# Kernel tuning notes

Hardware: AMD Instinct MI355X
Metric: run time of the kernel (lower is better)

The kernel has to match this reference:

```python
import jax, jax.numpy as jnp
import numpy as np

DIM = 1024
DIM_MEDIA = 1024
DIM_HEAD = 64
HEADS = 8
INNER = DIM_HEAD * HEADS  # 512
B, N_TOK, N_LAT = 4, 4096, 1024
LN_EPS = 1e-5


def setup_inputs() -> dict:
    key = jax.random.key(0)
    ks = jax.random.split(key, 6)
    x = jax.random.normal(ks[0], (B, N_TOK, DIM), dtype=jnp.float32)
    media = jax.random.normal(ks[1], (B, N_LAT, DIM_MEDIA), dtype=jnp.float32)
    media_mask = jax.random.randint(ks[2], (B, N_LAT), 0, 2).astype(bool)
    media_mask = media_mask.at[:, 0].set(True)  # avoid fully-masked rows (NaN softmax)
    ln_gamma = jnp.ones((DIM,), jnp.float32)
    ln_beta = jnp.zeros((DIM,), jnp.float32)
    Wq = jax.random.normal(ks[3], (DIM, INNER), jnp.float32) * (DIM ** -0.5)
    Wkv = jax.random.normal(ks[4], (DIM_MEDIA, 2 * INNER), jnp.float32) * (DIM_MEDIA ** -0.5)
    Wout = jax.random.normal(ks[5], (INNER, DIM), jnp.float32) * (INNER ** -0.5)
    return {"x": x, "media": media, "media_mask": media_mask,
            "ln_gamma": ln_gamma, "ln_beta": ln_beta,
            "Wq": Wq, "Wkv": Wkv, "Wout": Wout}


def reference(x, media, media_mask, ln_gamma, ln_beta, Wq, Wkv, Wout):
    scale = DIM_HEAD ** -0.5
    # LayerNorm over last dim
    mu = jnp.mean(x, axis=-1, keepdims=True)
    var = jnp.mean(jnp.square(x - mu), axis=-1, keepdims=True)
    xn = (x - mu) * jax.lax.rsqrt(var + LN_EPS) * ln_gamma + ln_beta

    q = (xn @ Wq) * scale                      # [b, n, inner]
    kv = media @ Wkv                           # [b, m, 2*inner]
    k, v = jnp.split(kv, 2, axis=-1)

    def to_heads(t):
        b, n, _ = t.shape
        return t.reshape(b, n, HEADS, DIM_HEAD).transpose(0, 2, 1, 3)  # b h n d

    q, k, v = to_heads(q), to_heads(k), to_heads(v)

    sim = jnp.einsum('bhid,bhjd->bhij', q, k)  # [b, h, n_tok, n_lat]
    neg_inf = jnp.float32(-jnp.inf)
    sim = jnp.where(media_mask[:, None, None, :], sim, neg_inf)
    sim = sim - jax.lax.stop_gradient(jnp.max(sim, axis=-1, keepdims=True))
    attn = jax.nn.softmax(sim, axis=-1)
    out = jnp.einsum('bhij,bhjd->bhid', attn, v)  # [b, h, n_tok, d]
    out = out.transpose(0, 2, 1, 3).reshape(out.shape[0], out.shape[2], INNER)
    return out @ Wout  # [b, n_tok, dim]
```

## Files before the change

kernel.cpp:

```cpp
#include <hip/hip_runtime.h>
#include <hip/hip_bf16.h>

typedef short bf16x8 __attribute__((ext_vector_type(8)));
typedef float f32x4 __attribute__((ext_vector_type(4)));
typedef unsigned short u16;

#define AS1 __attribute__((address_space(1)))
#define AS3 __attribute__((address_space(3)))

#define DIM     1024
#define INNER   512
#define HEADS   8
#define DHEAD   64
#define BATCH   4
#define NTOK    4096
#define NLAT    1024
#define M_X     (BATCH*NTOK)
#define M_MED   (BATCH*NLAT)
#define LN_EPS  1e-5f
#define QSCALE  (0.125f * 1.44269504f)

__device__ __forceinline__ float b2f(u16 h) {
    union { unsigned u; float f; } v; v.u = ((unsigned)h) << 16; return v.f;
}
__device__ __forceinline__ u16 f2b(float f) {
    union { float f; unsigned u; } v; v.f = f;
    unsigned r = v.u + 0x7fff + ((v.u >> 16) & 1);
    return (u16)(r >> 16);
}
__device__ __forceinline__ unsigned cvt_pk(float lo, float hi) {
    unsigned r;
    asm("v_cvt_pk_bf16_f32 %0, %1, %2" : "=v"(r) : "v"(lo), "v"(hi));
    return r;
}

__launch_bounds__(256)
__global__ void detect_kernel(const unsigned* __restrict__ xw, const unsigned* __restrict__ maskw,
                              unsigned* __restrict__ flags) {
    __shared__ int s_bad, s_byte;
    if (threadIdx.x == 0) { s_bad = 0; s_byte = 0; }
    __syncthreads();
    unsigned w = xw[threadIdx.x];
    int bad = 0;
    #pragma unroll
    for (int h = 0; h < 2; h++) {
        unsigned el = (h ? (w >> 16) : w) & 0xFFFFu;
        unsigned ef = (el >> 7) & 0xFFu;
        if (!((ef >= 64u && ef < 192u) || (el & 0x7FFFu) == 0u)) bad = 1;
    }
    if (bad) atomicOr(&s_bad, 1);
    for (int i = threadIdx.x; i < NLAT; i += 256)
        if (maskw[i] > 1u) { atomicOr(&s_byte, 1); break; }
    __syncthreads();
    if (threadIdx.x == 0) { flags[0] = s_bad ? 0u : 1u; flags[1] = s_byte ? 1u : 0u; }
}

#define PREP_BLOCKS 6156

__device__ __forceinline__ void do_transpose(const void* in, u16* out, int R, int C,
                                             int bx, int by, bool bf, u16 (*t)[33],
                                             const void* gv) {
    int c0 = bx * 32, r0 = by * 32;
    int tid = threadIdx.x;
    int r = tid >> 3, cb = (tid & 7) * 4;
    size_t base = (size_t)(r0 + r) * C + c0 + cb;
    u16 e0, e1, e2, e3;
    if (bf) {
        ushort4 a = *(const ushort4*)((const u16*)in + base);
        if (gv) {
            float sc = b2f(((const u16*)gv)[r0 + r]);
            e0 = f2b(b2f(a.x) * sc); e1 = f2b(b2f(a.y) * sc);
            e2 = f2b(b2f(a.z) * sc); e3 = f2b(b2f(a.w) * sc);
        } else {
            e0 = a.x; e1 = a.y; e2 = a.z; e3 = a.w;
        }
    } else {
        float4 a = *(const float4*)((const float*)in + base);
        float sc = gv ? ((const float*)gv)[r0 + r] : 1.f;
        e0 = f2b(a.x * sc); e1 = f2b(a.y * sc); e2 = f2b(a.z * sc); e3 = f2b(a.w * sc);
    }
    t[r][cb] = e0; t[r][cb + 1] = e1; t[r][cb + 2] = e2; t[r][cb + 3] = e3;
    __syncthreads();
    ushort4 o;
    o.x = t[cb + 0][r]; o.y = t[cb + 1][r]; o.z = t[cb + 2][r]; o.w = t[cb + 3][r];
    *(ushort4*)(out + (size_t)(c0 + r) * R + r0 + cb) = o;
}

__launch_bounds__(256)
__global__ void prep_kernel(const void* __restrict__ x, const void* __restrict__ g,
                            const void* __restrict__ bt, u16* __restrict__ xc,
                            const void* __restrict__ media, u16* __restrict__ media_c,
                            const void* __restrict__ mask, int* __restrict__ map,
                            int* __restrict__ cnt,
                            const void* __restrict__ Wq, u16* __restrict__ WqT,
                            const void* __restrict__ Wkv, u16* __restrict__ WkvT,
                            const void* __restrict__ Wout, u16* __restrict__ WoutT,
                            float2* __restrict__ stats, float* __restrict__ Gv,
                            float* __restrict__ Bv,
                            const unsigned* __restrict__ flags) {
    __shared__ int wsumI[4];
    __shared__ u16 t[32][33];
    __shared__ float rg[4][64], rb[4][64];
    bool bf = flags[0] != 0;
    int bid = blockIdx.x, tid = threadIdx.x;

    if (bid < 2048) {
        int w = tid >> 6, lane = tid & 63;
        int row0 = (bid << 3) + (w << 1);
        float v[2][16];
        if (bf) {
            const u16* xr = (const u16*)x + (size_t)row0 * DIM;
            bf16x8 a[4];
            #pragma unroll
            for (int rr = 0; rr < 2; rr++)
                #pragma unroll
                for (int i = 0; i < 2; i++)
                    a[rr * 2 + i] = *(const bf16x8*)(xr + (size_t)rr * DIM + (lane + 64 * i) * 8);
            #pragma unroll
            for (int rr = 0; rr < 2; rr++)
                #pragma unroll
                for (int i = 0; i < 2; i++)
                    #pragma unroll
                    for (int j = 0; j < 8; j++)
                        v[rr][i * 8 + j] = b2f((u16)a[rr * 2 + i][j]);
        } else {
            const float* xr = (const float*)x + (size_t)row0 * DIM;
            float4 a[8];
            #pragma unroll
            for (int rr = 0; rr < 2; rr++)
                #pragma unroll
                for (int i = 0; i < 4; i++)
                    a[rr * 4 + i] = *(const float4*)(xr + (size_t)rr * DIM + (lane + 64 * i) * 4);
            #pragma unroll
            for (int rr = 0; rr < 2; rr++)
                #pragma unroll
                for (int i = 0; i < 4; i++) {
                    v[rr][i * 4 + 0] = a[rr * 4 + i].x; v[rr][i * 4 + 1] = a[rr * 4 + i].y;
                    v[rr][i * 4 + 2] = a[rr * 4 + i].z; v[rr][i * 4 + 3] = a[rr * 4 + i].w;
                }
        }
        float s[2] = {0.f, 0.f}, s2[2] = {0.f, 0.f};
        #pragma unroll
        for (int rr = 0; rr < 2; rr++)
            #pragma unroll
            for (int i = 0; i < 16; i++) { s[rr] += v[rr][i]; s2[rr] += v[rr][i] * v[rr][i]; }
        #pragma unroll
        for (int m = 1; m < 64; m <<= 1) {
            #pragma unroll
            for (int rr = 0; rr < 2; rr++) {
                s[rr] += __shfl_xor(s[rr], m);
                s2[rr] += __shfl_xor(s2[rr], m);
            }
        }
        #pragma unroll
        for (int rr = 0; rr < 2; rr++) {
            float mu = s[rr] * (1.f / DIM);
            float var = s2[rr] * (1.f / DIM) - mu * mu;
            float inv = rsqrtf(fmaxf(var, 0.f) + LN_EPS);
            if (lane == 0) stats[row0 + rr] = make_float2(inv * QSCALE, inv * mu * QSCALE);
        }
        if (!bf) {
            u16* orow = xc + (size_t)row0 * DIM;
            #pragma unroll
            for (int rr = 0; rr < 2; rr++)
                #pragma unroll
                for (int i = 0; i < 4; i++) {
                    ushort4 o;
                    o.x = f2b(v[rr][i * 4 + 0]); o.y = f2b(v[rr][i * 4 + 1]);
                    o.z = f2b(v[rr][i * 4 + 2]); o.w = f2b(v[rr][i * 4 + 3]);
                    *(ushort4*)(orow + (size_t)rr * DIM + (lane + 64 * i) * 4) = o;
                }
        }
    } else if (bid < 4096) {
        if (bf) return;
        size_t i = ((size_t)(bid - 2048) * 256 + tid) * 8;
        const float* s = (const float*)media + i;
        float4 a = *(const float4*)s, b = *(const float4*)(s + 4);
        u16 o[8] = {f2b(a.x), f2b(a.y), f2b(a.z), f2b(a.w),
                    f2b(b.x), f2b(b.y), f2b(b.z), f2b(b.w)};
        *(bf16x8*)(media_c + i) = *(bf16x8*)o;
    } else if (bid < 4100) {
        int b = bid - 4096;
        bool bytes = flags[1] != 0;
        int v[4];
        if (bytes) {
            unsigned wd = ((const unsigned*)mask)[b * 256 + tid];
            #pragma unroll
            for (int i = 0; i < 4; i++) v[i] = ((wd >> (8 * i)) & 0xFFu) ? 1 : 0;
        } else {
            int4 m4 = ((const int4*)mask)[b * 256 + tid];
            v[0] = m4.x != 0; v[1] = m4.y != 0; v[2] = m4.z != 0; v[3] = m4.w != 0;
        }
        int tsum = v[0] + v[1] + v[2] + v[3];
        int lane = tid & 63, w = tid >> 6;
        int incl = tsum;
        #pragma unroll
        for (int off = 1; off < 64; off <<= 1) {
            int tt = __shfl_up(incl, off);
            if (lane >= off) incl += tt;
        }
        if (lane == 63) wsumI[w] = incl;
        __syncthreads();
        int base = 0;
        for (int k = 0; k < w; k++) base += wsumI[k];
        int slot = base + incl - tsum;
        int gbase = b * NLAT + tid * 4;
        #pragma unroll
        for (int i = 0; i < 4; i++) map[gbase + i] = v[i] ? slot++ : -1;
        if (tid == 0) cnt[b] = wsumI[0] + wsumI[1] + wsumI[2] + wsumI[3];
    } else if (bid < 4612) {
        int idx = bid - 4100;
        do_transpose(Wq, WqT, DIM, INNER, idx & 15, idx >> 4, bf, t, g);
    } else if (bid < 5636) {
        int idx = bid - 4612;
        do_transpose(Wkv, WkvT, DIM, DIM, idx & 31, idx >> 5, bf, t, nullptr);
    } else if (bid < 6148) {
        int idx = bid - 5636;
        do_transpose(Wout, WoutT, INNER, DIM, idx & 31, idx >> 5, bf, t, nullptr);
    } else {
        int idx = bid - 6148;
        int col = idx * 64 + (tid & 63), kq = tid >> 6;
        float ag = 0.f, ab = 0.f;
        if (bf) {
            const u16* W = (const u16*)Wq;
            const u16* gg = (const u16*)g;
            const u16* bb = (const u16*)bt;
            for (int k = kq * 256; k < kq * 256 + 256; k += 4) {
                #pragma unroll
                for (int u = 0; u < 4; u++) {
                    float wv = b2f(W[(size_t)(k + u) * INNER + col]);
                    ag += b2f(gg[k + u]) * wv;
                    ab += b2f(bb[k + u]) * wv;
                }
            }
        } else {
            const float* W = (const float*)Wq;
            const float* gg = (const float*)g;
            const float* bb = (const float*)bt;
            for (int k = kq * 256; k < kq * 256 + 256; k += 4) {
                #pragma unroll
                for (int u = 0; u < 4; u++) {
                    float wv = W[(size_t)(k + u) * INNER + col];
                    ag += gg[k + u] * wv;
                    ab += bb[k + u] * wv;
                }
            }
        }
        rg[kq][tid & 63] = ag; rb[kq][tid & 63] = ab;
        __syncthreads();
        if (kq == 0) {
            int c = tid & 63;
            Gv[col] = rg[0][c] + rg[1][c] + rg[2][c] + rg[3][c];
            Bv[col] = (rb[0][c] + rb[1][c] + rb[2][c] + rb[3][c]) * QSCALE;
        }
    }
}

__device__ __forceinline__ void gemm_body(const u16* __restrict__ A, const u16* __restrict__ Bt,
                                          u16* __restrict__ C, float* __restrict__ Cf,
                                          int Ndim, int K, float scale, int mode,
                                          u16* __restrict__ vT, const int* __restrict__ map,
                                          bool outbf, int n0, int m0, u16* As, u16* Bs,
                                          const float2* __restrict__ stats,
                                          const float* __restrict__ Gv,
                                          const float* __restrict__ Bv) {
    int tid = threadIdx.x;
    int w = tid >> 6, lane = tid & 63, quad = lane >> 4, l15 = lane & 15;
    int wm = (w >> 1) * 64, wn = (w & 1) * 64;
    f32x4 acc[4][4] = {};
    int rowInSeg = lane >> 2;
    int colB = (((lane & 3) ^ ((lane >> 3) & 3))) * 8;
    for (int k0 = 0; k0 < K; k0 += 32) {
        __syncthreads();
        #pragma unroll
        for (int i = 0; i < 2; i++) {
            int seg = w * 2 + i;
            int row = seg * 16 + rowInSeg;
            __builtin_amdgcn_global_load_lds(
                (const AS1 void*)(A + (size_t)(m0 + row) * K + k0 + colB),
                (AS3 void*)(As + seg * 512), 16, 0, 0);
            __builtin_amdgcn_global_load_lds(
                (const AS1 void*)(Bt + (size_t)(n0 + row) * K + k0 + colB),
                (AS3 void*)(Bs + seg * 512), 16, 0, 0);
        }
        __syncthreads();
        int sw = quad ^ ((l15 >> 1) & 3);
        bf16x8 af[4], bfr[4];
        #pragma unroll
        for (int i = 0; i < 4; i++)
            af[i] = *(bf16x8*)&As[(wm + i * 16 + l15) * 32 + sw * 8];
        #pragma unroll
        for (int j = 0; j < 4; j++)
            bfr[j] = *(bf16x8*)&Bs[(wn + j * 16 + l15) * 32 + sw * 8];
        #pragma unroll
        for (int i = 0; i < 4; i++)
            #pragma unroll
            for (int j = 0; j < 4; j++)
                acc[i][j] = __builtin_amdgcn_mfma_f32_16x16x32_bf16(af[i], bfr[j], acc[i][j], 0, 0, 0);
    }
    #pragma unroll
    for (int i = 0; i < 4; i++)
        #pragma unroll
        for (int j = 0; j < 4; j++)
            #pragma unroll
            for (int r = 0; r < 4; r++) {
                int row = m0 + wm + i * 16 + quad * 4 + r;
                int col = n0 + wn + j * 16 + l15;
                if (mode == 0) {
                    float2 st = stats[row];
                    float val = st.x * acc[i][j][r] - st.y * Gv[col] + Bv[col];
                    C[(size_t)row * Ndim + col] = f2b(val);
                } else if (mode == 1) {
                    float val = acc[i][j][r];
                    int b = row >> 10, jj = row & 1023;
                    int slot = map[(b << 10) + jj];
                    if (slot >= 0) {
                        if (col < INNER) {
                            C[((size_t)(b << 10) + slot) * INNER + col] = f2b(val);
                        } else {
                            int c = col - INNER;
                            int h = c >> 6, d = c & 63;
                            vT[(((size_t)(b * HEADS + h) * 64 + d) << 10) + slot] = f2b(val);
                        }
                    }
                } else {
                    float val = acc[i][j][r] * scale;
                    if (outbf) C[(size_t)row * Ndim + col] = f2b(val);
                    else       Cf[(size_t)row * Ndim + col] = val;
                }
            }
}

__launch_bounds__(256, 3)
__global__ void gemm128(const u16* __restrict__ A, const u16* __restrict__ Bt,
                        u16* __restrict__ C, float* __restrict__ Cf, int Ndim, int K,
                        float scale, int mode, u16* __restrict__ vT,
                        const int* __restrict__ map,
                        const unsigned* __restrict__ flags) {
    __shared__ __align__(16) u16 As[128 * 32];
    __shared__ __align__(16) u16 Bs[128 * 32];
    bool outbf = (mode != 2) || (flags[0] != 0);
    gemm_body(A, Bt, C, Cf, Ndim, K, scale, mode, vT, map, outbf,
              blockIdx.x * 128, blockIdx.y * 128, As, Bs,
              (const float2*)nullptr, (const float*)nullptr, (const float*)nullptr);
}

__launch_bounds__(256, 3)
__global__ void gemm_qkv(const void* __restrict__ x, const u16* __restrict__ xc,
                         const u16* __restrict__ WqT, u16* __restrict__ qb,
                         const void* __restrict__ media, const u16* __restrict__ media_c,
                         const u16* __restrict__ WkvT,
                         u16* __restrict__ Kb, u16* __restrict__ vT,
                         const int* __restrict__ map,
                         const float2* __restrict__ stats, const float* __restrict__ Gv,
                         const float* __restrict__ Bv,
                         const unsigned* __restrict__ flags) {
    __shared__ __align__(16) u16 As[128 * 32];
    __shared__ __align__(16) u16 Bs[128 * 32];
    bool bf = flags[0] != 0;
    int bid = blockIdx.x;
    if (bid < 512) {
        const u16* A = bf ? (const u16*)x : xc;
        gemm_body(A, WqT, qb, (float*)nullptr, INNER, DIM, 1.0f, 0,
                  (u16*)nullptr, (int*)nullptr, true,
                  (bid & 3) * 128, (bid >> 2) * 128, As, Bs, stats, Gv, Bv);
    } else {
        int id = bid - 512;
        const u16* A = bf ? (const u16*)media : media_c;
        gemm_body(A, WkvT, Kb, (float*)nullptr, DIM, DIM, 1.0f, 1,
                  vT, map, true,
                  (id & 7) * 128, (id >> 3) * 128, As, Bs,
                  (const float2*)nullptr, (const float*)nullptr, (const float*)nullptr);
    }
}

__launch_bounds__(256, 6)
__global__ void flash_kernel(const u16* __restrict__ q, const u16* __restrict__ Kc,
                             const u16* __restrict__ vTc, const int* __restrict__ cntp,
                             u16* __restrict__ attn_out) {
    __shared__ __align__(16) u16 Ks[64 * 64];
    __shared__ __align__(16) u16 Vts[64 * 64];
    __shared__ __align__(16) u16 Ps[4][16 * 68];
    int bh = blockIdx.x >> 6;
    int qt = blockIdx.x & 63;
    int b = bh >> 3, h = bh & 7;
    int tid = threadIdx.x, w = tid >> 6, lane = tid & 63, quad = lane >> 4, l15 = lane & 15;
    int qrow0 = qt * 64 + w * 16;
    int cnt = cntp[b];

    size_t qbase = ((size_t)(b * NTOK) + qrow0 + l15) * INNER + h * 64;
    bf16x8 qf[2];
    qf[0] = *(const bf16x8*)(q + qbase + quad * 8);
    qf[1] = *(const bf16x8*)(q + qbase + 32 + quad * 8);

    f32x4 Oacc[4] = {};
    float lsum = 0.f;
    int ld_row = lane >> 3;
    int ld_col = ((lane & 7) ^ ld_row) * 8;

    for (int jt = 0; jt < cnt; jt += 64) {
        __syncthreads();
        #pragma unroll
        for (int i = 0; i < 2; i++) {
            int seg = w * 2 + i;
            int j = jt + seg * 8 + ld_row;
            __builtin_amdgcn_global_load_lds(
                (const AS1 void*)(Kc + ((size_t)(b * NLAT) + j) * INNER + h * 64 + ld_col),
                (AS3 void*)(Ks + seg * 512), 16, 0, 0);
            int d = seg * 8 + ld_row;
            __builtin_amdgcn_global_load_lds(
                (const AS1 void*)(vTc + (((size_t)(b * HEADS + h) * 64 + d) << 10) + jt + ld_col),
                (AS3 void*)(Vts + seg * 512), 16, 0, 0);
        }
        __syncthreads();

        int sw0 = (quad ^ (l15 & 7)) * 8;
        int sw1 = ((quad + 4) ^ (l15 & 7)) * 8;
        f32x4 S[4];
        #pragma unroll
        for (int c = 0; c < 4; c++) {
            bf16x8 kf0 = *(bf16x8*)&Ks[(c * 16 + l15) * 64 + sw0];
            bf16x8 kf1 = *(bf16x8*)&Ks[(c * 16 + l15) * 64 + sw1];
            f32x4 s = {};
            s = __builtin_amdgcn_mfma_f32_16x16x32_bf16(kf0, qf[0], s, 0, 0, 0);
            s = __builtin_amdgcn_mfma_f32_16x16x32_bf16(kf1, qf[1], s, 0, 0, 0);
            S[c] = s;
        }
        if (jt + 64 <= cnt) {
            #pragma unroll
            for (int c = 0; c < 4; c++) {
                float p0 = exp2f(fminf(S[c][0], 115.4f));
                float p1 = exp2f(fminf(S[c][1], 115.4f));
                float p2 = exp2f(fminf(S[c][2], 115.4f));
                float p3 = exp2f(fminf(S[c][3], 115.4f));
                lsum += (p0 + p1) + (p2 + p3);
                uint2 pw = {cvt_pk(p0, p1), cvt_pk(p2, p3)};
                *(uint2*)&Ps[w][l15 * 68 + c * 16 + quad * 4] = pw;
            }
        } else {
            #pragma unroll
            for (int c = 0; c < 4; c++) {
                int kbase = jt + c * 16 + quad * 4;
                float p[4];
                #pragma unroll
                for (int r = 0; r < 4; r++) {
                    bool valid = (kbase + r) < cnt;
                    p[r] = valid ? exp2f(fminf(S[c][r], 115.4f)) : 0.f;
                    lsum += p[r];
                }
                uint2 pw = {cvt_pk(p[0], p[1]), cvt_pk(p[2], p[3])};
                *(uint2*)&Ps[w][l15 * 68 + c * 16 + quad * 4] = pw;
            }
        }
        asm volatile("s_waitcnt lgkmcnt(0)" ::: "memory");
        bf16x8 pf0 = *(bf16x8*)&Ps[w][l15 * 68 + quad * 8];
        bf16x8 pf1 = *(bf16x8*)&Ps[w][l15 * 68 + 32 + quad * 8];
        #pragma unroll
        for (int dt = 0; dt < 4; dt++) {
            bf16x8 vf0 = *(bf16x8*)&Vts[(dt * 16 + l15) * 64 + sw0];
            bf16x8 vf1 = *(bf16x8*)&Vts[(dt * 16 + l15) * 64 + sw1];
            Oacc[dt] = __builtin_amdgcn_mfma_f32_16x16x32_bf16(pf0, vf0, Oacc[dt], 0, 0, 0);
            Oacc[dt] = __builtin_amdgcn_mfma_f32_16x16x32_bf16(pf1, vf1, Oacc[dt], 0, 0, 0);
        }
    }
    lsum += __shfl_xor(lsum, 16);
    lsum += __shfl_xor(lsum, 32);
    #pragma unroll
    for (int r = 0; r < 4; r++) {
        float l = __shfl(lsum, quad * 4 + r);
        float invl = (l > 0.f) ? (1.f / l) : 0.f;
        #pragma unroll
        for (int dt = 0; dt < 4; dt++) {
            int row = qrow0 + quad * 4 + r;
            int col = h * 64 + dt * 16 + l15;
            attn_out[(size_t)(b * NTOK + row) * INNER + col] = f2b(Oacc[dt][r] * invl);
        }
    }
}

extern "C" void kernel_launch(void* const* d_in, const int* in_sizes, int n_in,
                              void* d_out, int out_size, void* d_ws, size_t ws_size,
                              hipStream_t stream) {
    const void* x     = d_in[0];
    const void* media = d_in[1];
    const void* mask  = d_in[2];
    const void* g     = d_in[3];
    const void* beta  = d_in[4];
    const void* Wq    = d_in[5];
    const void* Wkv   = d_in[6];
    const void* Wout  = d_in[7];

    char* ws = (char*)d_ws;
    unsigned* flags = (unsigned*)ws;   ws += 256;
    int* map_c  = (int*)ws;            ws += (size_t)M_MED * 4;
    int* cnt_c  = (int*)ws;            ws += 256;
    float2* stats = (float2*)ws;       ws += (size_t)M_X * 8;
    float* Gv   = (float*)ws;          ws += INNER * 4;
    float* Bv   = (float*)ws;          ws += INNER * 4;
    u16* media_c = (u16*)ws;           ws += (size_t)M_MED * DIM * 2;
    u16* xc    = (u16*)ws;             ws += (size_t)M_X * DIM * 2;
    u16* qb    = (u16*)ws;             ws += (size_t)M_X * INNER * 2;
    u16* Kb    = (u16*)ws;             ws += (size_t)M_MED * INNER * 2;
    u16* vTb   = (u16*)ws;             ws += (size_t)M_MED * INNER * 2;
    u16* ao    = (u16*)ws;             ws += (size_t)M_X * INNER * 2;
    u16* WqT   = (u16*)ws;             ws += (size_t)DIM * INNER * 2;
    u16* WkvT  = (u16*)ws;             ws += (size_t)DIM * DIM * 2;
    u16* WoutT = (u16*)ws;             ws += (size_t)INNER * DIM * 2;

    detect_kernel<<<1, 256, 0, stream>>>((const unsigned*)x, (const unsigned*)mask, flags);
    prep_kernel<<<PREP_BLOCKS, 256, 0, stream>>>(x, g, beta, xc, media, media_c, mask, map_c, cnt_c,
                                                 Wq, WqT, Wkv, WkvT, Wout, WoutT,
                                                 stats, Gv, Bv, flags);
    gemm_qkv<<<dim3(768), 256, 0, stream>>>(x, xc, WqT, qb, media, media_c, WkvT, Kb, vTb,
                                            map_c, stats, Gv, Bv, flags);
    flash_kernel<<<dim3(32 * 64), 256, 0, stream>>>(qb, Kb, vTb, cnt_c, ao);
    gemm128<<<dim3(DIM / 128, M_X / 128), 256, 0, stream>>>(ao, WoutT, (u16*)d_out, (float*)d_out, DIM, INNER,
                                                            1.0f, 2, (u16*)nullptr, (int*)nullptr, flags);
}
```

Before: 274.4 us.

## Fuse fp32-to-bf16 input conversion into QKV GEMM and widen K tile to 64

Removes the prep-stage passes that wrote bf16 copies of x and media. The QKV GEMM now reads fp32 activations directly, converts them in registers and stores them to a swizzled LDS tile. The GEMM K-step also grows from 32 to 64 with a new XOR swizzle, which halves the number of barrier pairs per tile but doubles LDS use per block. The fp32 A path uses plain vector loads instead of async global-to-LDS loads, so those loads may expose more latency.

```diff
diff --git a/kernel.cpp b/kernel.cpp
--- a/kernel.cpp
+++ b/kernel.cpp
@@ -55,7 +55,7 @@
     if (threadIdx.x == 0) { flags[0] = s_bad ? 0u : 1u; flags[1] = s_byte ? 1u : 0u; }
 }
 
-#define PREP_BLOCKS 6156
+#define PREP_BLOCKS 4108
 
 __device__ __forceinline__ void do_transpose(const void* in, u16* out, int R, int C,
                                              int bx, int by, bool bf, u16 (*t)[33],
@@ -88,8 +88,7 @@
 
 __launch_bounds__(256)
 __global__ void prep_kernel(const void* __restrict__ x, const void* __restrict__ g,
-                            const void* __restrict__ bt, u16* __restrict__ xc,
-                            const void* __restrict__ media, u16* __restrict__ media_c,
+                            const void* __restrict__ bt,
                             const void* __restrict__ mask, int* __restrict__ map,
                             int* __restrict__ cnt,
                             const void* __restrict__ Wq, u16* __restrict__ WqT,
@@ -107,43 +106,31 @@
     if (bid < 2048) {
         int w = tid >> 6, lane = tid & 63;
         int row0 = (bid << 3) + (w << 1);
-        float v[2][16];
+        float s[2] = {0.f, 0.f}, s2[2] = {0.f, 0.f};
         if (bf) {
             const u16* xr = (const u16*)x + (size_t)row0 * DIM;
-            bf16x8 a[4];
             #pragma unroll
             for (int rr = 0; rr < 2; rr++)
                 #pragma unroll
-                for (int i = 0; i < 2; i++)
-                    a[rr * 2 + i] = *(const bf16x8*)(xr + (size_t)rr * DIM + (lane + 64 * i) * 8);
-            #pragma unroll
-            for (int rr = 0; rr < 2; rr++)
-                #pragma unroll
-                for (int i = 0; i < 2; i++)
+                for (int i = 0; i < 2; i++) {
+                    bf16x8 a = *(const bf16x8*)(xr + (size_t)rr * DIM + (lane + 64 * i) * 8);
                     #pragma unroll
-                    for (int j = 0; j < 8; j++)
-                        v[rr][i * 8 + j] = b2f((u16)a[rr * 2 + i][j]);
+                    for (int j = 0; j < 8; j++) {
+                        float f = b2f((u16)a[j]);
+                        s[rr] += f; s2[rr] += f * f;
+                    }
+                }
         } else {
             const float* xr = (const float*)x + (size_t)row0 * DIM;
-            float4 a[8];
-            #pragma unroll
-            for (int rr = 0; rr < 2; rr++)
-                #pragma unroll
-                for (int i = 0; i < 4; i++)
-                    a[rr * 4 + i] = *(const float4*)(xr + (size_t)rr * DIM + (lane + 64 * i) * 4);
             #pragma unroll
             for (int rr = 0; rr < 2; rr++)
                 #pragma unroll
                 for (int i = 0; i < 4; i++) {
-                    v[rr][i * 4 + 0] = a[rr * 4 + i].x; v[rr][i * 4 + 1] = a[rr * 4 + i].y;
-                    v[rr][i * 4 + 2] = a[rr * 4 + i].z; v[rr][i * 4 + 3] = a[rr * 4 + i].w;
+                    float4 a = *(const float4*)(xr + (size_t)rr * DIM + (lane + 64 * i) * 4);
+                    s[rr] += a.x + a.y + a.z + a.w;
+                    s2[rr] += a.x * a.x + a.y * a.y + a.z * a.z + a.w * a.w;
                 }
         }
-        float s[2] = {0.f, 0.f}, s2[2] = {0.f, 0.f};
-        #pragma unroll
-        for (int rr = 0; rr < 2; rr++)
-            #pragma unroll
-            for (int i = 0; i < 16; i++) { s[rr] += v[rr][i]; s2[rr] += v[rr][i] * v[rr][i]; }
         #pragma unroll
         for (int m = 1; m < 64; m <<= 1) {
             #pragma unroll
@@ -159,28 +146,8 @@
             float inv = rsqrtf(fmaxf(var, 0.f) + LN_EPS);
             if (lane == 0) stats[row0 + rr] = make_float2(inv * QSCALE, inv * mu * QSCALE);
         }
-        if (!bf) {
-            u16* orow = xc + (size_t)row0 * DIM;
-            #pragma unroll
-            for (int rr = 0; rr < 2; rr++)
-                #pragma unroll
-                for (int i = 0; i < 4; i++) {
-                    ushort4 o;
-                    o.x = f2b(v[rr][i * 4 + 0]); o.y = f2b(v[rr][i * 4 + 1]);
-                    o.z = f2b(v[rr][i * 4 + 2]); o.w = f2b(v[rr][i * 4 + 3]);
-                    *(ushort4*)(orow + (size_t)rr * DIM + (lane + 64 * i) * 4) = o;
-                }
-        }
-    } else if (bid < 4096) {
-        if (bf) return;
-        size_t i = ((size_t)(bid - 2048) * 256 + tid) * 8;
-        const float* s = (const float*)media + i;
-        float4 a = *(const float4*)s, b = *(const float4*)(s + 4);
-        u16 o[8] = {f2b(a.x), f2b(a.y), f2b(a.z), f2b(a.w),
-                    f2b(b.x), f2b(b.y), f2b(b.z), f2b(b.w)};
-        *(bf16x8*)(media_c + i) = *(bf16x8*)o;
-    } else if (bid < 4100) {
-        int b = bid - 4096;
+    } else if (bid < 2052) {
+        int b = bid - 2048;
         bool bytes = flags[1] != 0;
         int v[4];
         if (bytes) {
@@ -208,17 +175,17 @@
         #pragma unroll
         for (int i = 0; i < 4; i++) map[gbase + i] = v[i] ? slot++ : -1;
         if (tid == 0) cnt[b] = wsumI[0] + wsumI[1] + wsumI[2] + wsumI[3];
-    } else if (bid < 4612) {
-        int idx = bid - 4100;
+    } else if (bid < 2564) {
+        int idx = bid - 2052;
         do_transpose(Wq, WqT, DIM, INNER, idx & 15, idx >> 4, bf, t, g);
-    } else if (bid < 5636) {
-        int idx = bid - 4612;
+    } else if (bid < 3588) {
+        int idx = bid - 2564;
         do_transpose(Wkv, WkvT, DIM, DIM, idx & 31, idx >> 5, bf, t, nullptr);
-    } else if (bid < 6148) {
-        int idx = bid - 5636;
+    } else if (bid < 4100) {
+        int idx = bid - 3588;
         do_transpose(Wout, WoutT, INNER, DIM, idx & 31, idx >> 5, bf, t, nullptr);
     } else {
-        int idx = bid - 6148;
+        int idx = bid - 4100;
         int col = idx * 64 + (tid & 63), kq = tid >> 6;
         float ag = 0.f, ab = 0.f;
         if (bf) {
@@ -256,7 +223,8 @@
     }
 }
 
-__device__ __forceinline__ void gemm_body(const u16* __restrict__ A, const u16* __restrict__ Bt,
+template<bool AF32>
+__device__ __forceinline__ void gemm_body(const void* __restrict__ Ap, const u16* __restrict__ Bt,
                                           u16* __restrict__ C, float* __restrict__ Cf,
                                           int Ndim, int K, float scale, int mode,
                                           u16* __restrict__ vT, const int* __restrict__ map,
@@ -268,35 +236,67 @@
     int w = tid >> 6, lane = tid & 63, quad = lane >> 4, l15 = lane & 15;
     int wm = (w >> 1) * 64, wn = (w & 1) * 64;
     f32x4 acc[4][4] = {};
-    int rowInSeg = lane >> 2;
-    int colB = (((lane & 3) ^ ((lane >> 3) & 3))) * 8;
-    for (int k0 = 0; k0 < K; k0 += 32) {
+    for (int k0 = 0; k0 < K; k0 += 64) {
         __syncthreads();
         #pragma unroll
-        for (int i = 0; i < 2; i++) {
-            int seg = w * 2 + i;
-            int row = seg * 16 + rowInSeg;
+        for (int i = 0; i < 4; i++) {
+            int slot = i * 256 + tid;
+            int row = slot >> 3;
+            int lg = (slot & 7) ^ (row & 7);
+            int wbase = (i * 256 + (tid & 192)) * 8;
             __builtin_amdgcn_global_load_lds(
-                (const AS1 void*)(A + (size_t)(m0 + row) * K + k0 + colB),
-                (AS3 void*)(As + seg * 512), 16, 0, 0);
-            __builtin_amdgcn_global_load_lds(
-                (const AS1 void*)(Bt + (size_t)(n0 + row) * K + k0 + colB),
-                (AS3 void*)(Bs + seg * 512), 16, 0, 0);
+                (const AS1 void*)(Bt + (size_t)(n0 + row) * K + k0 + lg * 8),
+                (AS3 void*)(Bs + wbase), 16, 0, 0);
+        }
+        if constexpr (AF32) {
+            int row = tid >> 1, ch = (tid & 1) * 32;
+            const float* src = (const float*)Ap + (size_t)(m0 + row) * K + k0 + ch;
+            float4 a[8];
+            #pragma unroll
+            for (int i = 0; i < 8; i++) a[i] = *(const float4*)(src + i * 4);
+            #pragma unroll
+            for (int gi = 0; gi < 4; gi++) {
+                int lg = (ch >> 3) + gi;
+                int ph = lg ^ (row & 7);
+                uint4 wv;
+                wv.x = cvt_pk(a[gi * 2].x, a[gi * 2].y);
+                wv.y = cvt_pk(a[gi * 2].z, a[gi * 2].w);
+                wv.z = cvt_pk(a[gi * 2 + 1].x, a[gi * 2 + 1].y);
+                wv.w = cvt_pk(a[gi * 2 + 1].z, a[gi * 2 + 1].w);
+                *(uint4*)&As[row * 64 + ph * 8] = wv;
+            }
+        } else {
+            #pragma unroll
+            for (int i = 0; i < 4; i++) {
+                int slot = i * 256 + tid;
+                int row = slot >> 3;
+                int lg = (slot & 7) ^ (row & 7);
+                int wbase = (i * 256 + (tid & 192)) * 8;
+                __builtin_amdgcn_global_load_lds(
+                    (const AS1 void*)((const u16*)Ap + (size_t)(m0 + row) * K + k0 + lg * 8),
+                    (AS3 void*)(As + wbase), 16, 0, 0);
+            }
         }
         __syncthreads();
-        int sw = quad ^ ((l15 >> 1) & 3);
-        bf16x8 af[4], bfr[4];
-        #pragma unroll
-        for (int i = 0; i < 4; i++)
-            af[i] = *(bf16x8*)&As[(wm + i * 16 + l15) * 32 + sw * 8];
-        #pragma unroll
-        for (int j = 0; j < 4; j++)
-            bfr[j] = *(bf16x8*)&Bs[(wn + j * 16 + l15) * 32 + sw * 8];
-        #pragma unroll
-        for (int i = 0; i < 4; i++)
-            #pragma unroll
-            for (int j = 0; j < 4; j++)
-                acc[i][j] = __builtin_amdgcn_mfma_f32_16x16x32_bf16(af[i], bfr[j], acc[i][j], 0, 0, 0);
+        #pragma unroll
+        for (int h = 0; h < 2; h++) {
+            bf16x8 af[4], bfr[4];
+            #pragma unroll
+            for (int i = 0; i < 4; i++) {
+                int R = wm + i * 16 + l15;
+                af[i] = *(bf16x8*)&As[R * 64 + (((quad + h * 4) ^ (R & 7)) * 8)];
+            }
+            #pragma unroll
+            for (int j = 0; j < 4; j++) {
+                int R = wn + j * 16 + l15;
+                bfr[j] = *(bf16x8*)&Bs[R * 64 + (((quad + h * 4) ^ (R & 7)) * 8)];
+            }
+            #pragma unroll
+            for (int i = 0; i < 4; i++)
+                #pragma unroll
+                for (int j = 0; j < 4; j++)
+                    acc[i][j] = __builtin_amdgcn_mfma_f32_16x16x32_bf16(af[i], bfr[j], acc[i][j], 0, 0, 0);
+        }
     }
     #pragma unroll
     for (int i = 0; i < 4; i++)
@@ -337,40 +337,46 @@
                         float scale, int mode, u16* __restrict__ vT,
                         const int* __restrict__ map,
                         const unsigned* __restrict__ flags) {
-    __shared__ __align__(16) u16 As[128 * 32];
-    __shared__ __align__(16) u16 Bs[128 * 32];
+    __shared__ __align__(16) u16 As[128 * 64];
+    __shared__ __align__(16) u16 Bs[128 * 64];
     bool outbf = (mode != 2) || (flags[0] != 0);
-    gemm_body(A, Bt, C, Cf, Ndim, K, scale, mode, vT, map, outbf,
-              blockIdx.x * 128, blockIdx.y * 128, As, Bs,
-              (const float2*)nullptr, (const float*)nullptr, (const float*)nullptr);
+    gemm_body<false>(A, Bt, C, Cf, Ndim, K, scale, mode, vT, map, outbf,
+                     blockIdx.x * 128, blockIdx.y * 128, As, Bs,
+                     (const float2*)nullptr, (const float*)nullptr, (const float*)nullptr);
 }
 
 __launch_bounds__(256, 3)
-__global__ void gemm_qkv(const void* __restrict__ x, const u16* __restrict__ xc,
-                         const u16* __restrict__ WqT, u16* __restrict__ qb,
-                         const void* __restrict__ media, const u16* __restrict__ media_c,
-                         const u16* __restrict__ WkvT,
+__global__ void gemm_qkv(const void* __restrict__ x, const u16* __restrict__ WqT,
+                         u16* __restrict__ qb,
+                         const void* __restrict__ media, const u16* __restrict__ WkvT,
                          u16* __restrict__ Kb, u16* __restrict__ vT,
                          const int* __restrict__ map,
                          const float2* __restrict__ stats, const float* __restrict__ Gv,
                          const float* __restrict__ Bv,
                          const unsigned* __restrict__ flags) {
-    __shared__ __align__(16) u16 As[128 * 32];
-    __shared__ __align__(16) u16 Bs[128 * 32];
+    __shared__ __align__(16) u16 As[128 * 64];
+    __shared__ __align__(16) u16 Bs[128 * 64];
     bool bf = flags[0] != 0;
     int bid = blockIdx.x;
     if (bid < 512) {
-        const u16* A = bf ? (const u16*)x : xc;
-        gemm_body(A, WqT, qb, (float*)nullptr, INNER, DIM, 1.0f, 0,
-                  (u16*)nullptr, (int*)nullptr, true,
-                  (bid & 3) * 128, (bid >> 2) * 128, As, Bs, stats, Gv, Bv);
+        int n0 = (bid & 3) * 128, m0 = (bid >> 2) * 128;
+        if (bf)
+            gemm_body<false>(x, WqT, qb, (float*)nullptr, INNER, DIM, 1.0f, 0,
+                             (u16*)nullptr, (int*)nullptr, true, n0, m0, As, Bs, stats, Gv, Bv);
+        else
+            gemm_body<true>(x, WqT, qb, (float*)nullptr, INNER, DIM, 1.0f, 0,
+                            (u16*)nullptr, (int*)nullptr, true, n0, m0, As, Bs, stats, Gv, Bv);
     } else {
         int id = bid - 512;
-        const u16* A = bf ? (const u16*)media : media_c;
-        gemm_body(A, WkvT, Kb, (float*)nullptr, DIM, DIM, 1.0f, 1,
-                  vT, map, true,
-                  (id & 7) * 128, (id >> 3) * 128, As, Bs,
-                  (const float2*)nullptr, (const float*)nullptr, (const float*)nullptr);
+        int n0 = (id & 7) * 128, m0 = (id >> 3) * 128;
+        if (bf)
+            gemm_body<false>(media, WkvT, Kb, (float*)nullptr, DIM, DIM, 1.0f, 1,
+                             vT, map, true, n0, m0, As, Bs,
+                             (const float2*)nullptr, (const float*)nullptr, (const float*)nullptr);
+        else
+            gemm_body<true>(media, WkvT, Kb, (float*)nullptr, DIM, DIM, 1.0f, 1,
+                            vT, map, true, n0, m0, As, Bs,
+                            (const float2*)nullptr, (const float*)nullptr, (const float*)nullptr);
     }
 }
 
@@ -497,8 +503,6 @@
     float2* stats = (float2*)ws;       ws += (size_t)M_X * 8;
     float* Gv   = (float*)ws;          ws += INNER * 4;
     float* Bv   = (float*)ws;          ws += INNER * 4;
-    u16* media_c = (u16*)ws;           ws += (size_t)M_MED * DIM * 2;
-    u16* xc    = (u16*)ws;             ws += (size_t)M_X * DIM * 2;
     u16* qb    = (u16*)ws;             ws += (size_t)M_X * INNER * 2;
     u16* Kb    = (u16*)ws;             ws += (size_t)M_MED * INNER * 2;
     u16* vTb   = (u16*)ws;             ws += (size_t)M_MED * INNER * 2;
@@ -508,10 +512,10 @@
     u16* WoutT = (u16*)ws;             ws += (size_t)INNER * DIM * 2;
 
     detect_kernel<<<1, 256, 0, stream>>>((const unsigned*)x, (const unsigned*)mask, flags);
-    prep_kernel<<<PREP_BLOCKS, 256, 0, stream>>>(x, g, beta, xc, media, media_c, mask, map_c, cnt_c,
+    prep_kernel<<<PREP_BLOCKS, 256, 0, stream>>>(x, g, beta, mask, map_c, cnt_c,
                                                  Wq, WqT, Wkv, WkvT, Wout, WoutT,
                                                  stats, Gv, Bv, flags);
-    gemm_qkv<<<dim3(768), 256, 0, stream>>>(x, xc, WqT, qb, media, media_c, WkvT, Kb, vTb,
+    gemm_qkv<<<dim3(768), 256, 0, stream>>>(x, WqT, qb, media, WkvT, Kb, vTb,
                                             map_c, stats, Gv, Bv, flags);
     flash_kernel<<<dim3(32 * 64), 256, 0, stream>>>(qb, Kb, vTb, cnt_c, ao);
     gemm128<<<dim3(DIM / 128, M_X / 128), 256, 0, stream>>>(ao, WoutT, (u16*)d_out, (float*)d_out, DIM, INNER,
```

After: 293.7 us. +7.0%, slower.
